# Kernel optimization log

Measured on AMD Instinct MI355X. Metric: run time of the kernel, lower is better.

The kernel has to match this reference:

```python
import jax, jax.numpy as jnp
import numpy as np

DIM = 1536
NH = 12
HD = DIM // NH          # 128
C = HD // 2             # 64 rotary pairs
F, H, W = 6, 20, 20
L = F * H * W           # 2400
B = 1
MAX_POS = 1024
EPS = 1e-6


def _rope_freqs():
    """[MAX_POS, C, 2, 2] rotation matrices, split [22,21,21] across f/h/w axes."""
    c0 = C - 2 * (C // 3)           # 22
    c1 = C // 3                      # 21
    pos = np.arange(MAX_POS, dtype=np.float32)
    parts = []
    for m in (c0, c1, c1):
        inv = 1.0 / (10000.0 ** (np.arange(m, dtype=np.float32) / m))
        parts.append(pos[:, None] * inv[None, :])
    ang = np.concatenate(parts, axis=1)          # [MAX_POS, C]
    cos, sin = np.cos(ang), np.sin(ang)
    # R[..., j, k]: rows [cos, -sin], [sin, cos]
    R = np.stack([np.stack([cos, -sin], -1), np.stack([sin, cos], -1)], -2)
    return jnp.asarray(R, dtype=jnp.float32)


def setup_inputs() -> dict:
    key = jax.random.key(0)
    ks = jax.random.split(key, 12)
    s = 1.0 / np.sqrt(DIM)
    lin = lambda k: (jax.random.normal(k, (DIM, DIM), jnp.float32) * s)
    return {
        "x": jax.random.normal(ks[0], (B, L, DIM), jnp.float32),
        "Wq": lin(ks[1]), "bq": jax.random.normal(ks[2], (DIM,), jnp.float32) * 0.01,
        "Wk": lin(ks[3]), "bk": jax.random.normal(ks[4], (DIM,), jnp.float32) * 0.01,
        "Wv": lin(ks[5]), "bv": jax.random.normal(ks[6], (DIM,), jnp.float32) * 0.01,
        "Wo": lin(ks[7]), "bo": jax.random.normal(ks[8], (DIM,), jnp.float32) * 0.01,
        "gq": jnp.ones((DIM,), jnp.float32),
        "gk": jnp.ones((DIM,), jnp.float32),
        "seq_lens": jnp.full((B,), L, dtype=jnp.int32),
        "grid_sizes": jnp.asarray([[F, H, W]], dtype=jnp.int32),
        "freqs": _rope_freqs(),
    }


def _rms_norm(x, g, eps=EPS):
    # WanRMSNorm: x * rsqrt(mean(x^2, -1) + eps) * weight
    return x * jax.lax.rsqrt(jnp.mean(jnp.square(x), axis=-1, keepdims=True) + eps) * g


def _rope_apply(xh, grid_sizes, freqs):
    """xh: [B, L, n, d]; freqs: [MAX_POS, c, 2, 2]. All samples share one grid."""
    b, l, n, d = xh.shape
    c = d // 2
    c0 = c - 2 * (c // 3)
    c1 = c // 3
    f, h, w = (int(v) for v in np.asarray(grid_sizes[0]))
    # build per-position 3D rotation matrices: [f*h*w, c, 2, 2]
    fa = jnp.broadcast_to(freqs[:f, :c0][:, None, None], (f, h, w, c0, 2, 2))
    fb = jnp.broadcast_to(freqs[:h, c0:c0 + c1][None, :, None], (f, h, w, c1, 2, 2))
    fc = jnp.broadcast_to(freqs[:w, c0 + c1:c][None, None, :], (f, h, w, c1, 2, 2))
    R = jnp.concatenate([fa, fb, fc], axis=3).reshape(f * h * w, c, 2, 2)
    xp = xh.reshape(b, l, n, c, 2)
    out = jnp.einsum('lcjk,blnck->blncj', R, xp)
    return out.reshape(b, l, n, d)


def reference(x, Wq, bq, Wk, bk, Wv, bv, Wo, bo, gq, gk, seq_lens, grid_sizes, freqs):
    b, l = x.shape[:2]
    q = _rms_norm(x @ Wq.T + bq, gq).reshape(b, l, NH, HD)
    k = _rms_norm(x @ Wk.T + bk, gk).reshape(b, l, NH, HD)
    v = (x @ Wv.T + bv).reshape(b, l, NH, HD)
    q = _rope_apply(q, grid_sizes, freqs)
    k = _rope_apply(k, grid_sizes, freqs)
    # full attention with key-length mask (window_size=(-1,-1))
    scores = jnp.einsum('bqnd,bknd->bnqk', q, k) / np.sqrt(HD)
    kmask = jnp.arange(l)[None, :] < seq_lens[:, None]          # [B, L]
    scores = jnp.where(kmask[:, None, None, :], scores, -1e9)
    attn = jax.nn.softmax(scores, axis=-1)
    out = jnp.einsum('bnqk,bknd->bqnd', attn, v).reshape(b, l, DIM)
    return out @ Wo.T + bo
```

## Files before the change

### kernel.cpp

```cpp
#include <hip/hip_runtime.h>
#include <hip/hip_bf16.h>
#include <stdint.h>


#define DIM  1536
#define NH   12
#define HD   128
#define LSEQ 2400
#define LPAD 2432
#define KT2  32
#define NT2  (LPAD / KT2)
#define NTQ  19

typedef __attribute__((ext_vector_type(8))) short short8;
typedef __attribute__((ext_vector_type(8))) _Float16 half8;
typedef __attribute__((ext_vector_type(4))) float f32x4;
typedef unsigned short ushort_t;
typedef unsigned int   uint32;

__device__ __forceinline__ ushort_t f2bf(float f) {
  union { float f; unsigned u; } v; v.f = f;
  unsigned r = (v.u + 0x7fffu + ((v.u >> 16) & 1u)) >> 16;
  return (ushort_t)r;
}
__device__ __forceinline__ float bf2f(ushort_t h) {
  union { unsigned u; float f; } v; v.u = ((unsigned)h) << 16;
  return v.f;
}
__device__ __forceinline__ void async16(void* lds, const void* g) {
  __builtin_amdgcn_global_load_lds(
      (const __attribute__((address_space(1))) uint32*)g,
      (__attribute__((address_space(3))) uint32*)lds, 16, 0, 0);
}
__device__ __forceinline__ uint4 pack8(const float* f) {
  uint4 u;
  u.x = (uint32)f2bf(f[0]) | ((uint32)f2bf(f[1]) << 16);
  u.y = (uint32)f2bf(f[2]) | ((uint32)f2bf(f[3]) << 16);
  u.z = (uint32)f2bf(f[4]) | ((uint32)f2bf(f[5]) << 16);
  u.w = (uint32)f2bf(f[6]) | ((uint32)f2bf(f[7]) << 16);
  return u;
}

__global__ void cvt_all(const float* __restrict__ x,
                        const float* __restrict__ W0, const float* __restrict__ W1,
                        const float* __restrict__ W2, const float* __restrict__ W3,
                        ushort_t* __restrict__ xd,
                        ushort_t* __restrict__ d0, ushort_t* __restrict__ d1,
                        ushort_t* __restrict__ d2, ushort_t* __restrict__ d3)
{
  const int z = blockIdx.y;
  const int i = blockIdx.x * 256 + threadIdx.x;
  if (z == 0) {
    uint4 u = {0, 0, 0, 0};
    if (i * 8 < LSEQ * DIM) {
      float f[8];
      *(float4*)f = *(const float4*)(x + i * 8);
      *(float4*)(f + 4) = *(const float4*)(x + i * 8 + 4);
      u = pack8(f);
    }
    *(uint4*)(xd + i * 8) = u;
    return;
  }
  if (blockIdx.x >= DIM * DIM / 2048) return;
  const float* s = (z == 1) ? W0 : ((z == 2) ? W1 : ((z == 3) ? W2 : W3));
  ushort_t* d    = (z == 1) ? d0 : ((z == 2) ? d1 : ((z == 3) ? d2 : d3));
  float f[8];
  *(float4*)f = *(const float4*)(s + i * 8);
  *(float4*)(f + 4) = *(const float4*)(s + i * 8 + 4);
  *(uint4*)(d + i * 8) = pack8(f);
}

template<int OUT_F32>
__global__ __launch_bounds__(256) void gemm_bt(
    const ushort_t* __restrict__ Ap,
    const ushort_t* __restrict__ B0, const ushort_t* __restrict__ B1, const ushort_t* __restrict__ B2,
    const float* __restrict__ b0, const float* __restrict__ b1, const float* __restrict__ b2,
    void* __restrict__ D0, void* __restrict__ D1, void* __restrict__ D2,
    int Mout)
{
  const int z = blockIdx.y;
  const ushort_t* Bw  = (z == 0) ? B0 : ((z == 1) ? B1 : B2);
  const float* bias   = (z == 0) ? b0 : ((z == 1) ? b1 : b2);
  void* D             = (z == 0) ? D0 : ((z == 1) ? D1 : D2);

  const int bm = blockIdx.x / 12, bn = blockIdx.x % 12;
  const int tid = threadIdx.x;
  const int w = tid >> 6, lam = tid & 63;
  const int wr = w >> 1, wc = w & 1;
  const int lane15 = lam & 15, quad = lam >> 4;

  __shared__ __align__(16) char lds[32768];
  char* sA = lds;
  char* sB = lds + 16384;

  f32x4 acc[4][4];
#pragma unroll
  for (int i = 0; i < 4; ++i)
#pragma unroll
    for (int j = 0; j < 4; ++j) acc[i][j] = {};

  const int sm = (w * 32) + (lam >> 3);
  const int sc = (lam & 7);

  for (int k0 = 0; k0 < DIM; k0 += 64) {
    __syncthreads();
#pragma unroll
    for (int i = 0; i < 4; ++i) {
      const int li = w * 4096 + i * 1024;
      const int m = sm + i * 8;
      const int c = sc ^ (m & 7);
      async16(sA + li, Ap + (size_t)(bm * 128 + m) * DIM + k0 + c * 8);
      async16(sB + li, Bw + (size_t)(bn * 128 + m) * DIM + k0 + c * 8);
    }
    __syncthreads();
#pragma unroll
    for (int kc = 0; kc < 2; ++kc) {
      const int chunk = kc * 4 + quad;
      short8 af[4], bfr[4];
#pragma unroll
      for (int i = 0; i < 4; ++i) {
        const int m = wr * 64 + i * 16 + lane15;
        af[i] = *(const short8*)(sA + m * 128 + ((chunk ^ (m & 7)) * 16));
      }
#pragma unroll
      for (int j = 0; j < 4; ++j) {
        const int n = wc * 64 + j * 16 + lane15;
        bfr[j] = *(const short8*)(sB + n * 128 + ((chunk ^ (n & 7)) * 16));
      }
#pragma unroll
      for (int i = 0; i < 4; ++i)
#pragma unroll
        for (int j = 0; j < 4; ++j)
          acc[i][j] = __builtin_amdgcn_mfma_f32_16x16x32_bf16(af[i], bfr[j], acc[i][j], 0, 0, 0);
    }
  }

#pragma unroll
  for (int j = 0; j < 4; ++j) {
    const int n = bn * 128 + wc * 64 + j * 16 + lane15;
    const float bv = bias[n];
#pragma unroll
    for (int i = 0; i < 4; ++i) {
      const int mb = bm * 128 + wr * 64 + i * 16 + quad * 4;
#pragma unroll
      for (int r = 0; r < 4; ++r) {
        const int m = mb + r;
        const float val = acc[i][j][r] + bv;
        if (OUT_F32) {
          if (m < Mout) ((float*)D)[(size_t)m * DIM + n] = val;
        } else {
          ((ushort_t*)D)[(size_t)m * DIM + n] = f2bf(val);
        }
      }
    }
  }
}

__global__ __launch_bounds__(256) void nr_vp(
    const ushort_t* __restrict__ qpre, const ushort_t* __restrict__ kpre,
    const ushort_t* __restrict__ vbf,
    const float* __restrict__ gq, const float* __restrict__ gk,
    const float* __restrict__ freqs,
    const int* __restrict__ seq_lens, const int* __restrict__ grid_sizes,
    ushort_t* __restrict__ qh, ushort_t* __restrict__ kh,
    ushort_t* __restrict__ vp)
{
  const int bx = blockIdx.x;
  const int tid = threadIdx.x;
  __shared__ float wsum[4];
  __shared__ float srstd;
  __shared__ ushort_t tbuf[32][33];

  if (bx >= 2 * LPAD) {
    const int vb = bx - 2 * LPAD;
    const int head = vb / (NT2 * 4);
    const int rem = vb - head * (NT2 * 4);
    const int t2 = rem >> 2;
    const int d0 = (rem & 3) * 32;
    const int l0 = t2 * 32;
    const int tx = tid & 31, ty = tid >> 5;
#pragma unroll
    for (int rr = 0; rr < 4; ++rr)
      tbuf[ty * 4 + rr][tx] = vbf[(size_t)(l0 + ty * 4 + rr) * DIM + head * HD + d0 + tx];
    __syncthreads();
    const int tx2 = ((tx >> 2) & 3) * 8 + (tx >> 4) * 4 + (tx & 3);
#pragma unroll
    for (int rr = 0; rr < 4; ++rr) {
      const int d = d0 + ty * 4 + rr;
      vp[(((size_t)head * NT2 + t2) * HD + d) * KT2 + tx2] = tbuf[tx][ty * 4 + rr];
    }
    return;
  }

  const int row = bx >> 1;
  const int which = bx & 1;
  const ushort_t* src = which ? kpre : qpre;
  const float* g = which ? gk : gq;
  ushort_t* dst = which ? kh : qh;

  float s = 0.f;
  if (tid < 192) {
    uint4 u = *(const uint4*)(src + (size_t)row * DIM + tid * 8);
    const uint32 uu[4] = {u.x, u.y, u.z, u.w};
#pragma unroll
    for (int i = 0; i < 4; ++i) {
      float a = bf2f((ushort_t)(uu[i] & 0xffff));
      float b = bf2f((ushort_t)(uu[i] >> 16));
      s += a * a + b * b;
    }
  }
#pragma unroll
  for (int off = 32; off; off >>= 1) s += __shfl_down(s, off, 64);
  if ((tid & 63) == 0) wsum[tid >> 6] = s;
  __syncthreads();
  if (tid == 0)
    srstd = rsqrtf((wsum[0] + wsum[1] + wsum[2] + wsum[3]) / (float)DIM + 1e-6f);
  __syncthreads();
  const float rstd = srstd;

  const int seq = seq_lens[0];
  const int h_ = grid_sizes[1], w_ = grid_sizes[2];
  const int hw = h_ * w_;
  const int fidx = row / hw;
  const int rem = row - fidx * hw;
  const int hidx = rem / w_;
  const int widx = rem - hidx * w_;
  const bool live = row < seq;

#pragma unroll
  for (int pp = 0; pp < 3; ++pp) {
    const int p = tid + pp * 256;
    const int c = p & 63, head = p >> 6;
    const int e_in = head * HD + 2 * c;
    uint32 xin = *(const uint32*)(src + (size_t)row * DIM + e_in);
    float x0 = bf2f((ushort_t)(xin & 0xffff));
    float x1 = bf2f((ushort_t)(xin >> 16));
    float2 gg = *(const float2*)(g + e_in);
    float y0 = x0 * rstd * gg.x, y1 = x1 * rstd * gg.y;
    const int pos = (c < 22) ? fidx : ((c < 43) ? hidx : widx);
    float4 R = *(const float4*)(freqs + ((size_t)pos * 64 + c) * 4);
    float o0 = R.x * y0 + R.y * y1;
    float o1 = R.z * y0 + R.w * y1;
    uint32 op = live ? ((uint32)f2bf(o0) | ((uint32)f2bf(o1) << 16)) : 0u;
    *(uint32*)(dst + ((size_t)head * LPAD + row) * HD + 2 * c) = op;
  }
}

__global__ __launch_bounds__(256, 3) void attn8(
    const ushort_t* __restrict__ qh, const ushort_t* __restrict__ kh,
    const ushort_t* __restrict__ vp, const int* __restrict__ seq_lens,
    _Float16* __restrict__ op0, _Float16* __restrict__ op1,
    _Float16* __restrict__ op2, _Float16* __restrict__ op3,
    float* __restrict__ lp)
{
  const int qz = blockIdx.z;
  const int head = blockIdx.y;
  const int q0 = blockIdx.x * 128;
  const int tid = threadIdx.x;
  const int w = tid >> 6, lam = tid & 63;
  const int lane15 = lam & 15, quad = lam >> 4;
  const int seq = seq_lens[0];
  _Float16* op = (qz == 0) ? op0 : ((qz == 1) ? op1 : ((qz == 2) ? op2 : op3));

  __shared__ __align__(16) char kbuf[2][8192];
  __shared__ __align__(16) char vbuf[2][8192];

  const ushort_t* qbase = qh + ((size_t)head * LPAD + q0 + w * 32) * HD;
  short8 qf[2][4];
#pragma unroll
  for (int qt = 0; qt < 2; ++qt)
#pragma unroll
    for (int kc = 0; kc < 4; ++kc)
      qf[qt][kc] = *(const short8*)(qbase + (qt * 16 + lane15) * HD + kc * 32 + quad * 8);

  f32x4 o[2][8];
#pragma unroll
  for (int qt = 0; qt < 2; ++qt)
#pragma unroll
    for (int dt = 0; dt < 8; ++dt) o[qt][dt] = {};
  float lacc[2] = {};

  const float c1 = 0.12751744510848893f;
  const float c2 = 17.312340490667562f;

  const ushort_t* khh = kh + (size_t)head * LPAD * HD;
  const ushort_t* vph = vp + (size_t)head * NT2 * HD * KT2;

  const int krow0 = w * 8 + (lam >> 4);
  const int kslot = lam & 15;

#define STAGE(gt, b)                                                     \
  {                                                                      \
    const ushort_t* kg = khh + (size_t)(gt) * (KT2 * HD);                \
    const ushort_t* vg = vph + (size_t)(gt) * (HD * KT2);                \
    _Pragma("unroll")                                                    \
    for (int i = 0; i < 2; ++i) {                                        \
      const int li = w * 2048 + i * 1024;                                \
      const int kr = krow0 + i * 4;                                      \
      const int kc_ = kslot ^ (kr & 15);                                 \
      async16(kbuf[b] + li, kg + kr * HD + kc_ * 8);                     \
      const int G = w * 128 + i * 64 + lam;                              \
      const int vdt = G >> 6, vdd = (G >> 2) & 15, vqq = G & 3;          \
      async16(vbuf[b] + li, vg + (vdt * 16 + vdd) * KT2 + vqq * 8);      \
    }                                                                    \
  }

  const int tbase = qz * NTQ;
  STAGE(tbase, 0)
  __syncthreads();

  for (int t = 0; t < NTQ; ++t) {
    const int b = t & 1;
    const int gt = tbase + t;
    if (t + 1 < NTQ) STAGE(gt + 1, b ^ 1)

    f32x4 S[2][2];
    S[0][0] = {}; S[0][1] = {}; S[1][0] = {}; S[1][1] = {};
#pragma unroll
    for (int n0 = 0; n0 < 2; ++n0)
#pragma unroll
      for (int kc = 0; kc < 4; ++kc) {
        short8 kf = *(const short8*)(kbuf[b] + (n0 * 16 + lane15) * 256 +
                                     (((kc * 4 + quad) ^ lane15) * 16));
#pragma unroll
        for (int qt = 0; qt < 2; ++qt)
          S[qt][n0] = __builtin_amdgcn_mfma_f32_16x16x32_bf16(kf, qf[qt][kc], S[qt][n0], 0, 0, 0);
      }

    short8 pa8[2];
#pragma unroll
    for (int qt = 0; qt < 2; ++qt) {
      float ev[8];
      float s8 = 0.f;
#pragma unroll
      for (int n0 = 0; n0 < 2; ++n0) {
        const int kb0 = gt * KT2 + n0 * 16 + quad * 4;
#pragma unroll
        for (int r = 0; r < 4; ++r) {
          float e = (kb0 + r < seq) ? exp2f(S[qt][n0][r] * c1 - c2) : 0.f;
          ev[n0 * 4 + r] = e;
          s8 += e;
        }
      }
      lacc[qt] += s8;
      union { uint32 u[4]; short8 s; } pk;
#pragma unroll
      for (int p = 0; p < 4; ++p)
        pk.u[p] = (uint32)f2bf(ev[2 * p]) | ((uint32)f2bf(ev[2 * p + 1]) << 16);
      pa8[qt] = pk.s;
    }

#pragma unroll
    for (int dt = 0; dt < 8; ++dt) {
      short8 vf = *(const short8*)(vbuf[b] + dt * 1024 + lane15 * 64 + quad * 16);
#pragma unroll
      for (int qt = 0; qt < 2; ++qt)
        o[qt][dt] = __builtin_amdgcn_mfma_f32_16x16x32_bf16(pa8[qt], vf, o[qt][dt], 0, 0, 0);
    }
    __syncthreads();
  }
#undef STAGE

#pragma unroll
  for (int qt = 0; qt < 2; ++qt) {
    float l = lacc[qt];
    l += __shfl_xor(l, 16, 64);
    l += __shfl_xor(l, 32, 64);
    if (lam < 16)
      lp[((size_t)qz * NH + head) * LPAD + q0 + w * 32 + qt * 16 + lam] = l;
    const float lrcp = 1.0f / l;
    float linv[4];
#pragma unroll
    for (int r = 0; r < 4; ++r) linv[r] = __shfl(lrcp, quad * 4 + r, 64);
#pragma unroll
    for (int dt = 0; dt < 8; ++dt)
#pragma unroll
      for (int r = 0; r < 4; ++r) {
        const int m = q0 + w * 32 + qt * 16 + quad * 4 + r;
        op[(size_t)m * DIM + head * HD + dt * 16 + lane15] =
            (_Float16)(o[qt][dt][r] * linv[r]);
      }
  }
}

__global__ void merge(const _Float16* __restrict__ o0, const _Float16* __restrict__ o1,
                      const _Float16* __restrict__ o2, const _Float16* __restrict__ o3,
                      const float* __restrict__ lp, ushort_t* __restrict__ attno)
{
  const int i = blockIdx.x * 256 + threadIdx.x;
  const int e = i * 8;
  const int m = e / DIM;
  const int head = (e - m * DIM) >> 7;
  float l[4];
#pragma unroll
  for (int h = 0; h < 4; ++h) l[h] = lp[((size_t)h * NH + head) * LPAD + m];
  const float inv = 1.0f / (l[0] + l[1] + l[2] + l[3]);
  half8 a = *(const half8*)(o0 + e);
  half8 b = *(const half8*)(o1 + e);
  half8 c = *(const half8*)(o2 + e);
  half8 d = *(const half8*)(o3 + e);
  const float w0 = l[0] * inv, w1 = l[1] * inv, w2 = l[2] * inv, w3 = l[3] * inv;
  float f[8];
#pragma unroll
  for (int j = 0; j < 8; ++j)
    f[j] = (float)a[j] * w0 + (float)b[j] * w1 + (float)c[j] * w2 + (float)d[j] * w3;
  *(uint4*)(attno + e) = pack8(f);
}

extern "C" void kernel_launch(void* const* d_in, const int* in_sizes, int n_in,
                              void* d_out, int out_size, void* d_ws, size_t ws_size,
                              hipStream_t stream)
{
  const float* x  = (const float*)d_in[0];
  const float* Wq = (const float*)d_in[1];
  const float* bq = (const float*)d_in[2];
  const float* Wk = (const float*)d_in[3];
  const float* bk = (const float*)d_in[4];
  const float* Wv = (const float*)d_in[5];
  const float* bv = (const float*)d_in[6];
  const float* Wo = (const float*)d_in[7];
  const float* bo = (const float*)d_in[8];
  const float* gq = (const float*)d_in[9];
  const float* gk = (const float*)d_in[10];
  const int* seq_lens   = (const int*)d_in[11];
  const int* grid_sizes = (const int*)d_in[12];
  const float* freqs    = (const float*)d_in[13];
  float* out = (float*)d_out;

  const size_t BUF = (size_t)LPAD * DIM * 2;
  const size_t WB  = (size_t)DIM * DIM * 2;
  char* ws = (char*)d_ws;
  dim3 blk(256);

  ushort_t* xbf  = (ushort_t*)(ws);
  ushort_t* wqb  = (ushort_t*)(ws + BUF);
  ushort_t* wkb  = (ushort_t*)(ws + BUF + WB);
  ushort_t* wvb  = (ushort_t*)(ws + BUF + 2 * WB);
  ushort_t* wob  = (ushort_t*)(ws + BUF + 3 * WB);
  ushort_t* qpre = (ushort_t*)(ws + BUF + 4 * WB);
  ushort_t* kpre = (ushort_t*)(ws + 2 * BUF + 4 * WB);
  ushort_t* qh   = (ushort_t*)(ws + 3 * BUF + 4 * WB);
  ushort_t* kh   = (ushort_t*)(ws + 4 * BUF + 4 * WB);
  ushort_t* vbf  = (ushort_t*)(ws + 5 * BUF + 4 * WB);
  ushort_t* vp    = xbf;
  ushort_t* attno = xbf;
  _Float16* op0 = (_Float16*)qpre;
  _Float16* op1 = (_Float16*)kpre;
  _Float16* op2 = (_Float16*)vbf;
  _Float16* op3 = (_Float16*)wqb;
  float*    lp  = (float*)wvb;

  cvt_all<<<dim3(LPAD * DIM / 2048, 5), blk, 0, stream>>>(
      x, Wq, Wk, Wv, Wo, xbf, wqb, wkb, wvb, wob);
  gemm_bt<0><<<dim3(228, 3), blk, 0, stream>>>(
      xbf, wqb, wkb, wvb, bq, bk, bv, qpre, kpre, vbf, 0);
  nr_vp<<<dim3(2 * LPAD + NH * NT2 * 4), blk, 0, stream>>>(
      qpre, kpre, vbf, gq, gk, freqs, seq_lens, grid_sizes, qh, kh, vp);
  attn8<<<dim3(LPAD / 128, NH, 4), blk, 0, stream>>>(
      qh, kh, vp, seq_lens, op0, op1, op2, op3, lp);
  merge<<<dim3(LPAD * DIM / 2048), blk, 0, stream>>>(op0, op1, op2, op3, lp, attno);
  gemm_bt<1><<<dim3(228, 1), blk, 0, stream>>>(
      attno, wob, wob, wob, bo, bo, bo, out, out, out, LSEQ);
}
```

Baseline: 293.9 us.

## Swizzle block order for XCD locality and streamline softmax masking and bf16 packing

New measurement: 287.8 us. -2.1%, faster.

```diff
diff --git a/kernel.cpp b/kernel.cpp
--- a/kernel.cpp
+++ b/kernel.cpp
@@ -26,6 +26,11 @@
 __device__ __forceinline__ float bf2f(ushort_t h) {
   union { unsigned u; float f; } v; v.u = ((unsigned)h) << 16;
   return v.f;
+}
+__device__ __forceinline__ uint32 cvtpk(float lo, float hi) {
+  uint32 r;
+  asm("v_cvt_pk_bf16_f32 %0, %1, %2" : "=v"(r) : "v"(lo), "v"(hi));
+  return r;
 }
 __device__ __forceinline__ void async16(void* lds, const void* g) {
   __builtin_amdgcn_global_load_lds(
@@ -83,7 +88,10 @@
   const float* bias   = (z == 0) ? b0 : ((z == 1) ? b1 : b2);
   void* D             = (z == 0) ? D0 : ((z == 1) ? D1 : D2);
 
-  const int bm = blockIdx.x / 12, bn = blockIdx.x % 12;
+  const int bid = blockIdx.x;
+  const int x_ = bid & 7, k_ = bid >> 3;
+  const int swz = (x_ < 4 ? x_ * 29 : 116 + (x_ - 4) * 28) + k_;
+  const int bm = swz / 12, bn = swz % 12;
   const int tid = threadIdx.x;
   const int w = tid >> 6, lam = tid & 63;
   const int wr = w >> 1, wc = w & 1;
@@ -253,9 +261,13 @@
     _Float16* __restrict__ op2, _Float16* __restrict__ op3,
     float* __restrict__ lp)
 {
-  const int qz = blockIdx.z;
-  const int head = blockIdx.y;
-  const int q0 = blockIdx.x * 128;
+  const int bid = blockIdx.x;
+  const int swz = (bid & 7) * 114 + (bid >> 3);
+  const int qx = swz % 19;
+  const int rest = swz / 19;
+  const int head = rest % 12;
+  const int qz = rest / 12;
+  const int q0 = qx * 128;
   const int tid = threadIdx.x;
   const int w = tid >> 6, lam = tid & 63;
   const int lane15 = lam & 15, quad = lam >> 4;
@@ -327,26 +339,33 @@
           S[qt][n0] = __builtin_amdgcn_mfma_f32_16x16x32_bf16(kf, qf[qt][kc], S[qt][n0], 0, 0, 0);
       }
 
+    const bool edge = (gt + 1) * KT2 > seq;
     short8 pa8[2];
 #pragma unroll
     for (int qt = 0; qt < 2; ++qt) {
       float ev[8];
-      float s8 = 0.f;
-#pragma unroll
-      for (int n0 = 0; n0 < 2; ++n0) {
-        const int kb0 = gt * KT2 + n0 * 16 + quad * 4;
-#pragma unroll
-        for (int r = 0; r < 4; ++r) {
-          float e = (kb0 + r < seq) ? exp2f(S[qt][n0][r] * c1 - c2) : 0.f;
-          ev[n0 * 4 + r] = e;
-          s8 += e;
+#pragma unroll
+      for (int n0 = 0; n0 < 2; ++n0)
+#pragma unroll
+        for (int r = 0; r < 4; ++r)
+          ev[n0 * 4 + r] = exp2f(S[qt][n0][r] * c1 - c2);
+      if (edge) {
+#pragma unroll
+        for (int n0 = 0; n0 < 2; ++n0) {
+          const int kb0 = gt * KT2 + n0 * 16 + quad * 4;
+#pragma unroll
+          for (int r = 0; r < 4; ++r)
+            if (kb0 + r >= seq) ev[n0 * 4 + r] = 0.f;
         }
       }
+      float s8 = ((ev[0] + ev[1]) + (ev[2] + ev[3])) +
+                 ((ev[4] + ev[5]) + (ev[6] + ev[7]));
       lacc[qt] += s8;
       union { uint32 u[4]; short8 s; } pk;
-#pragma unroll
-      for (int p = 0; p < 4; ++p)
-        pk.u[p] = (uint32)f2bf(ev[2 * p]) | ((uint32)f2bf(ev[2 * p + 1]) << 16);
+      pk.u[0] = cvtpk(ev[0], ev[1]);
+      pk.u[1] = cvtpk(ev[2], ev[3]);
+      pk.u[2] = cvtpk(ev[4], ev[5]);
+      pk.u[3] = cvtpk(ev[6], ev[7]);
       pa8[qt] = pk.s;
     }
 
@@ -456,7 +475,7 @@
       xbf, wqb, wkb, wvb, bq, bk, bv, qpre, kpre, vbf, 0);
   nr_vp<<<dim3(2 * LPAD + NH * NT2 * 4), blk, 0, stream>>>(
       qpre, kpre, vbf, gq, gk, freqs, seq_lens, grid_sizes, qh, kh, vp);
-  attn8<<<dim3(LPAD / 128, NH, 4), blk, 0, stream>>>(
+  attn8<<<dim3(912), blk, 0, stream>>>(
       qh, kh, vp, seq_lens, op0, op1, op2, op3, lp);
   merge<<<dim3(LPAD * DIM / 2048), blk, 0, stream>>>(op0, op1, op2, op3, lp, attno);
   gemm_bt<1><<<dim3(228, 1), blk, 0, stream>>>(
```
